# Performance work log

Measured on AMD Instinct MI355X. Metric: run time of the kernel, lower is better.

## Reference

```python
import jax, jax.numpy as jnp
import numpy as np

EMBED_DIMS = 256

def setup_inputs() -> dict:
    key = jax.random.key(0)
    ks = jax.random.split(key, 6)
    C = EMBED_DIMS
    x = jax.random.normal(ks[0], (4, 2048, C), dtype=jnp.float32)
    prev_x = jax.random.normal(ks[1], (4, 2048, C), dtype=jnp.float32)
    s = 1.0 / np.sqrt(C)
    W_qkv = jax.random.uniform(ks[2], (C, 3 * C), dtype=jnp.float32, minval=-s, maxval=s)
    b_qkv = jax.random.uniform(ks[3], (3 * C,), dtype=jnp.float32, minval=-s, maxval=s)
    W_out = jax.random.uniform(ks[4], (C, C), dtype=jnp.float32, minval=-s, maxval=s)
    b_out = jax.random.uniform(ks[5], (C,), dtype=jnp.float32, minval=-s, maxval=s)
    return {"x": x, "prev_x": prev_x, "W_qkv": W_qkv, "b_qkv": b_qkv,
            "W_out": W_out, "b_out": b_out}

def reference(x, prev_x, W_qkv, b_qkv, W_out, b_out):
    B, N, C = x.shape
    xx = jnp.concatenate([prev_x, x], axis=1)          # [B, S, C], S = 2N
    qkv = xx @ W_qkv + b_qkv                            # [B, S, 3C]
    q, k, v = jnp.split(qkv, 3, axis=-1)                # each [B, S, C]
    scale = 1.0 / jnp.sqrt(jnp.asarray(C, dtype=x.dtype))
    attn = jax.nn.softmax(jnp.einsum('bqc,bkc->bqk', q, k) * scale, axis=-1)
    out = jnp.einsum('bqk,bkc->bqc', attn, v)           # [B, S, C]
    out = out @ W_out + b_out
    return out[:, -N:, :]                               # [B, N, C]
```

## Files before the change

kernel.cpp:

```cpp
#include <hip/hip_runtime.h>

typedef __bf16 bf16;
typedef __attribute__((ext_vector_type(8))) __bf16 bf16x8;
typedef __attribute__((ext_vector_type(4))) __bf16 bf16x4;
typedef __attribute__((ext_vector_type(4))) float f32x4;
typedef __attribute__((ext_vector_type(16))) float f32x16;
typedef __attribute__((ext_vector_type(4))) unsigned u32x4;

#define MFMA16(a, b, c) __builtin_amdgcn_mfma_f32_16x16x32_bf16(a, b, c, 0, 0, 0)
#define MFMA32(a, b, c) __builtin_amdgcn_mfma_f32_32x32x16_bf16(a, b, c, 0, 0, 0)

__device__ inline void gload_lds16(const void* g, void* l) {
  __builtin_amdgcn_global_load_lds(
      (const __attribute__((address_space(1))) void*)g,
      (__attribute__((address_space(3))) void*)l, 16, 0, 0);
}

__device__ inline unsigned packbf(float a, float b) {
  unsigned short x = __builtin_bit_cast(unsigned short, (bf16)a);
  unsigned short y = __builtin_bit_cast(unsigned short, (bf16)b);
  return (unsigned)x | ((unsigned)y << 16);
}

__global__ __launch_bounds__(256) void prep_w_kernel(
    const float* __restrict__ Wqkv, const float* __restrict__ Wout,
    bf16* __restrict__ Wqkvt, bf16* __restrict__ Woutt)
{
  int tid = blockIdx.x * 256 + threadIdx.x;
  int nth = gridDim.x * 256;
  for (int i = tid; i < 768 * 256; i += nth) {
    int n = i >> 8, k = i & 255;
    Wqkvt[i] = (bf16)Wqkv[k * 768 + n];
  }
  for (int i = tid; i < 256 * 256; i += nth) {
    int n = i >> 8, k = i & 255;
    Woutt[i] = (bf16)Wout[k * 256 + n];
  }
}

__global__ __launch_bounds__(256) void gemm_qkv_kernel(
    const float* __restrict__ x, const float* __restrict__ px,
    const bf16* __restrict__ Wt, const float* __restrict__ bias,
    bf16* __restrict__ Qo, bf16* __restrict__ KVo)
{
  const int bi = blockIdx.x;
  const int b = bi >> 6;
  const int mblk = bi & 63;
  const bool mhalf = mblk >= 32;
  const int bm = b * 4096 + mblk * 64;
  const int s_local = (mblk & 31) * 64;
  const float* xsrc = mhalf ? x : px;
  const size_t xbase = ((size_t)b << 19) + (size_t)s_local * 256;

  const int tid = threadIdx.x;
  const int lane = tid & 63, w = tid >> 6;
  const int l15 = lane & 15, lg = lane >> 4;

  alignas(16) __shared__ bf16 Alds[64 * 256];
  alignas(16) __shared__ bf16 Wlds[2][256 * 32];

  const int ystart = mhalf ? 0 : 1;
  const int nseq = mhalf ? 24 : 16;

  auto stageW = [&](int i) {
    const int y = ystart + (i >> 3);
    const int k0 = (i & 7) * 32;
    #pragma unroll
    for (int jj = 0; jj < 4; jj++) {
      int j = w * 4 + jj;
      int row = j * 16 + (lane >> 2);
      int chunk = (lane & 3) ^ ((row >> 1) & 3);
      const bf16* g = Wt + (size_t)(y * 256 + row) * 256 + k0 + chunk * 8;
      gload_lds16(g, (char*)&Wlds[i & 1][0] + j * 1024);
    }
  };
  stageW(0);

  #pragma unroll
  for (int it = 0; it < 8; it++) {
    int c = it * 256 + tid;
    int row = c >> 5, ch = c & 31;
    const float* src = xsrc + xbase + (size_t)row * 256 + ch * 8;
    float4 f0 = *(const float4*)src;
    float4 f1 = *(const float4*)(src + 4);
    bf16x8 v = { (bf16)f0.x, (bf16)f0.y, (bf16)f0.z, (bf16)f0.w,
                 (bf16)f1.x, (bf16)f1.y, (bf16)f1.z, (bf16)f1.w };
    *(bf16x8*)((char*)Alds + ((c << 4) ^ ((row & 7) << 4))) = v;
  }
  __syncthreads();

  f32x4 acc[16] = {};
  for (int i = 0; i < nseq; i++) {
    if (i + 1 < nseq) stageW(i + 1);
    const int k0 = (i & 7) * 32;
    const bf16* wbuf = &Wlds[i & 1][0];
    const int arow = w * 16 + l15;
    bf16x8 afr = *(const bf16x8*)((char*)Alds +
        ((arow * 512 + k0 * 2 + lg * 16) ^ ((arow & 7) << 4)));
    #pragma unroll
    for (int nt = 0; nt < 16; nt++) {
      const int wrow = nt * 16 + l15;
      bf16x8 bfr = *(const bf16x8*)((char*)wbuf +
          (((wrow << 6) + (lg << 4)) ^ (((wrow >> 1) & 3) << 4)));
      acc[nt] = MFMA16(afr, bfr, acc[nt]);
    }
    __syncthreads();

    if ((i & 7) == 7) {
      const int y = ystart + (i >> 3);
      const int m0 = bm + w * 16 + lg * 4;
      const int bq = m0 >> 12, s = m0 & 4095;
      #pragma unroll
      for (int nt = 0; nt < 16; nt++) {
        const int n = nt * 16 + l15;
        const float bv = bias[y * 256 + n];
        if (y == 0) {
          const int ks = n >> 4, h2 = (n >> 3) & 1, e = n & 7;
          #pragma unroll
          for (int rr = 0; rr < 4; rr++) {
            const int qrow = bq * 2048 + (s - 2048) + rr;
            Qo[(size_t)(qrow >> 5) * 8192 + ks * 512 +
               ((qrow & 31) + 32 * h2) * 8 + e] =
                (bf16)((acc[nt][rr] + bv) * 0.0625f);
          }
        } else if (y == 1) {
          const int d = n;
          const int ks = d >> 4, h2 = (d >> 3) & 1, e = d & 7;
          const size_t tb = (size_t)(bq * 128 + (s >> 5)) * 16384;
          #pragma unroll
          for (int rr = 0; rr < 4; rr++)
            KVo[tb + ks * 512 + (((s & 31) + rr) + 32 * h2) * 8 + e] =
                (bf16)(acc[nt][rr] + bv);
        } else {
          const int d = n;
          const int kv32 = s & 31;
          const int sidx = kv32 >> 4, h2 = (kv32 >> 3) & 1, e0 = kv32 & 7;
          bf16x4 st = { (bf16)(acc[nt][0] + bv), (bf16)(acc[nt][1] + bv),
                        (bf16)(acc[nt][2] + bv), (bf16)(acc[nt][3] + bv) };
          *(bf16x4*)(KVo + (size_t)(bq * 128 + (s >> 5)) * 16384 + 8192 +
                     (sidx * 8 + (d >> 5)) * 512 + ((d & 31) + 32 * h2) * 8 + e0) = st;
        }
        acc[nt] = (f32x4){};
      }
    }
  }
}

__global__ __launch_bounds__(256, 2) void attn_kernel(
    const bf16* __restrict__ Qp, const bf16* __restrict__ KVp,
    bf16* __restrict__ Opart, float* __restrict__ ml)
{
  const int id = blockIdx.x;
  const int c = id & 7;
  const int b = (id >> 3) & 3;
  const int qb = id >> 5;
  const int tid = threadIdx.x;
  const int lane = tid & 63, w = tid >> 6;
  const int l31 = lane & 31, hi = lane >> 5;

  __shared__ bf16 lds[2][16384];

  const int qg = b * 64 + qb * 4 + w;
  const bf16* qbase = Qp + (size_t)qg * 8192 + lane * 8;
  bf16x8 qf[16];
  #pragma unroll
  for (int ks = 0; ks < 16; ks++)
    qf[ks] = *(const bf16x8*)(qbase + ks * 512);

  const bf16* kvtile0 = KVp + (size_t)(b * 128 + c * 16) * 16384;

  auto stage = [&](int t) {
    const char* g = (const char*)(kvtile0 + (size_t)t * 16384) + w * 8192 + lane * 16;
    char* l = (char*)&lds[t & 1][0] + w * 8192;
    #pragma unroll
    for (int j = 0; j < 8; j++)
      gload_lds16(g + j * 1024, l + j * 1024);
  };
  stage(0);

  f32x16 o[8] = {};
  float m_run = -1e30f, l_run = 0.f;

  for (int t = 0; t < 16; t++) {
    __syncthreads();
    if (t + 1 < 16) stage(t + 1);
    const bf16* kbuf = &lds[t & 1][0];
    const bf16* vbuf = kbuf + 8192;

    f32x16 p = {};
    __builtin_amdgcn_s_setprio(1);
    #pragma unroll
    for (int ks = 0; ks < 16; ks++) {
      bf16x8 kf = *(const bf16x8*)(kbuf + ks * 512 + lane * 8);
      p = MFMA32(kf, qf[ks], p);
    }
    __builtin_amdgcn_s_setprio(0);

    float mt = fmaxf(p[0], p[1]);
    #pragma unroll
    for (int i = 2; i < 16; i++) mt = fmaxf(mt, p[i]);
    mt = fmaxf(mt, __shfl_xor(mt, 32));
    if (!__all(mt <= m_run + 8.f)) {
      const float m_new = fmaxf(m_run, mt);
      const float alpha = __expf(m_run - m_new);
      l_run *= alpha;
      #pragma unroll
      for (int i = 0; i < 8; i++)
        #pragma unroll
        for (int j = 0; j < 16; j++) o[i][j] *= alpha;
      m_run = m_new;
    }
    float ps = 0.f;
    #pragma unroll
    for (int i = 0; i < 16; i++) { p[i] = __expf(p[i] - m_run); ps += p[i]; }
    ps += __shfl_xor(ps, 32);
    l_run += ps;

    unsigned u[8], xp[8];
    #pragma unroll
    for (int i = 0; i < 8; i++) u[i] = packbf(p[2 * i], p[2 * i + 1]);
    #pragma unroll
    for (int i = 0; i < 8; i++)
      xp[i] = (unsigned)__shfl_xor((int)u[i], 32);
    const u32x4 w0 = hi ? (u32x4){xp[2], xp[3], u[2], u[3]}
                        : (u32x4){u[0], u[1], xp[0], xp[1]};
    const u32x4 w1 = hi ? (u32x4){xp[6], xp[7], u[6], u[7]}
                        : (u32x4){u[4], u[5], xp[4], xp[5]};
    const bf16x8 pf0 = __builtin_bit_cast(bf16x8, w0);
    const bf16x8 pf1 = __builtin_bit_cast(bf16x8, w1);

    __builtin_amdgcn_s_setprio(1);
    #pragma unroll
    for (int dg = 0; dg < 8; dg++) {
      bf16x8 v0 = *(const bf16x8*)(vbuf + dg * 512 + lane * 8);
      o[dg] = MFMA32(v0, pf0, o[dg]);
      bf16x8 v1 = *(const bf16x8*)(vbuf + (8 + dg) * 512 + lane * 8);
      o[dg] = MFMA32(v1, pf1, o[dg]);
    }
    __builtin_amdgcn_s_setprio(0);
  }

  const int q = b * 2048 + qb * 128 + w * 32 + l31;
  bf16* ob = Opart + ((size_t)c * 8192 + q) * 256;
  #pragma unroll
  for (int dg = 0; dg < 8; dg++) {
    #pragma unroll
    for (int r4 = 0; r4 < 4; r4++) {
      const int d = dg * 32 + r4 * 8 + hi * 4;
      bf16x4 st = { (bf16)o[dg][r4 * 4 + 0], (bf16)o[dg][r4 * 4 + 1],
                    (bf16)o[dg][r4 * 4 + 2], (bf16)o[dg][r4 * 4 + 3] };
      *(bf16x4*)(ob + d) = st;
    }
  }
  if (hi == 0) {
    float2 v = { m_run, l_run };
    *(float2*)(ml + ((size_t)c * 8192 + q) * 2) = v;
  }
}

__global__ __launch_bounds__(256) void out_kernel(
    const bf16* __restrict__ Opart, const float* __restrict__ ml,
    const bf16* __restrict__ Woutt, const float* __restrict__ bout,
    float* __restrict__ out)
{
  const int bm = blockIdx.x * 32;
  const int tid = threadIdx.x;
  const int lane = tid & 63, w = tid >> 6;
  const int l15 = lane & 15, lg = lane >> 4;

  alignas(16) __shared__ bf16 Alds[32 * 256];
  alignas(16) __shared__ bf16 Wlds[2][256 * 32];

  auto stageW = [&](int k0) {
    #pragma unroll
    for (int jj = 0; jj < 4; jj++) {
      int j = w * 4 + jj;
      int row = j * 16 + (lane >> 2);
      int chunk = (lane & 3) ^ ((row >> 1) & 3);
      const bf16* g = Woutt + (size_t)row * 256 + k0 * 32 + chunk * 8;
      gload_lds16(g, (char*)&Wlds[k0 & 1][0] + j * 1024);
    }
  };
  stageW(0);

  #pragma unroll
  for (int ch = 0; ch < 4; ch++) {
    const int idx = ch * 256 + tid;
    const int row = idx >> 5;
    const int dc = (idx & 31) << 3;
    const int q = bm + row;
    float ms[8], ls[8], M = -1e30f;
    #pragma unroll
    for (int s = 0; s < 8; s++) {
      float2 v = *(const float2*)(ml + ((size_t)s * 8192 + q) * 2);
      ms[s] = v.x; ls[s] = v.y;
      M = fmaxf(M, v.x);
    }
    float L = 0.f, acc[8] = {};
    #pragma unroll
    for (int s = 0; s < 8; s++) {
      const float wgt = __expf(ms[s] - M);
      L += ls[s] * wgt;
      bf16x8 v = *(const bf16x8*)(Opart + ((size_t)s * 8192 + q) * 256 + dc);
      #pragma unroll
      for (int j = 0; j < 8; j++) acc[j] += wgt * (float)v[j];
    }
    const float inv = 1.f / L;
    bf16x8 st;
    #pragma unroll
    for (int j = 0; j < 8; j++) st[j] = (bf16)(acc[j] * inv);
    *(bf16x8*)((char*)Alds + ((row * 512 + dc * 2) ^ ((row & 7) << 4))) = st;
  }
  __syncthreads();

  f32x4 acc[8] = {};
  for (int k0 = 0; k0 < 8; k0++) {
    if (k0 + 1 < 8) stageW(k0 + 1);
    const bf16* wbuf = &Wlds[k0 & 1][0];
    const int arow = (w & 1) * 16 + l15;
    bf16x8 afr = *(const bf16x8*)((char*)Alds +
        ((arow * 512 + k0 * 64 + lg * 16) ^ ((arow & 7) << 4)));
    #pragma unroll
    for (int nt = 0; nt < 8; nt++) {
      const int wrow = (w >> 1) * 128 + nt * 16 + l15;
      bf16x8 bfr = *(const bf16x8*)((char*)wbuf +
          (((wrow << 6) + (lg << 4)) ^ (((wrow >> 1) & 3) << 4)));
      acc[nt] = MFMA16(afr, bfr, acc[nt]);
    }
    __syncthreads();
  }

  #pragma unroll
  for (int nt = 0; nt < 8; nt++) {
    const int n = (w >> 1) * 128 + nt * 16 + l15;
    const float bvv = bout[n];
    const int m0 = bm + (w & 1) * 16 + lg * 4;
    #pragma unroll
    for (int r = 0; r < 4; r++)
      out[(size_t)(m0 + r) * 256 + n] = acc[nt][r] + bvv;
  }
}

extern "C" void kernel_launch(void* const* d_in, const int* in_sizes, int n_in,
                              void* d_out, int out_size, void* d_ws, size_t ws_size,
                              hipStream_t stream) {
  const float* x    = (const float*)d_in[0];
  const float* px   = (const float*)d_in[1];
  const float* Wqkv = (const float*)d_in[2];
  const float* bqkv = (const float*)d_in[3];
  const float* Wout = (const float*)d_in[4];
  const float* bout = (const float*)d_in[5];
  float* out = (float*)d_out;

  char* ws = (char*)d_ws;
  bf16* Qp    = (bf16*)(ws);
  bf16* KVp   = (bf16*)(ws + 4194304);
  bf16* Woutt = (bf16*)(ws + 20971520);
  bf16* Wqkvt = (bf16*)(ws + 21102592);
  float* ml   = (float*)(ws + 21495808);
  bf16* Opart = (bf16*)(ws + 22020096);

  prep_w_kernel<<<dim3(128), dim3(256), 0, stream>>>(Wqkv, Wout, Wqkvt, Woutt);
  gemm_qkv_kernel<<<dim3(256), dim3(256), 0, stream>>>(
      x, px, Wqkvt, bqkv, Qp, KVp);
  attn_kernel<<<dim3(512), dim3(256), 0, stream>>>(Qp, KVp, Opart, ml);
  out_kernel<<<dim3(256), dim3(256), 0, stream>>>(Opart, ml, Woutt, bout, out);
}
```

Measured before the change: 104.7 us.

## Split QKV GEMM across output projections into 640 blocks with per-k staging

The QKV projection kernel used to launch one block per 64-row tile, and each block looped over two or three output projections (K,V or Q,K,V). Now each block handles one (row tile, projection) pair, giving 640 blocks and better balance across CUs. The A tile is loaded per 32-wide k slice instead of once for the full 256 width, and W is no longer double-buffered. LDS use drops, which may allow more resident blocks, but each block now re-reads and re-converts x for every projection and has no overlap between loads and MFMA.

```diff
diff --git a/kernel.cpp b/kernel.cpp
--- a/kernel.cpp
+++ b/kernel.cpp
@@ -43,105 +43,91 @@
     const bf16* __restrict__ Wt, const float* __restrict__ bias,
     bf16* __restrict__ Qo, bf16* __restrict__ KVo)
 {
-  const int bi = blockIdx.x;
-  const int b = bi >> 6;
-  const int mblk = bi & 63;
-  const bool mhalf = mblk >= 32;
+  const int idb = blockIdx.x;
+  const int b = idb / 160;
+  const int r = idb % 160;
+  int mblk, y;
+  if (r < 64) { mblk = r >> 1; y = 1 + (r & 1); }
+  else { int r2 = r - 64; mblk = 32 + r2 / 3; y = r2 % 3; }
   const int bm = b * 4096 + mblk * 64;
-  const int s_local = (mblk & 31) * 64;
-  const float* xsrc = mhalf ? x : px;
-  const size_t xbase = ((size_t)b << 19) + (size_t)s_local * 256;
 
   const int tid = threadIdx.x;
   const int lane = tid & 63, w = tid >> 6;
   const int l15 = lane & 15, lg = lane >> 4;
 
-  alignas(16) __shared__ bf16 Alds[64 * 256];
-  alignas(16) __shared__ bf16 Wlds[2][256 * 32];
-
-  const int ystart = mhalf ? 0 : 1;
-  const int nseq = mhalf ? 24 : 16;
-
-  auto stageW = [&](int i) {
-    const int y = ystart + (i >> 3);
-    const int k0 = (i & 7) * 32;
+  alignas(16) __shared__ bf16 Alds[64 * 32];
+  alignas(16) __shared__ bf16 Wlds[256 * 32];
+
+  f32x4 acc[16] = {};
+
+  const float* xsrc = (mblk >= 32) ? x : px;
+  const size_t xbase = ((size_t)b << 19) + (size_t)((mblk & 31) * 64) * 256;
+
+  for (int k0 = 0; k0 < 256; k0 += 32) {
+    __syncthreads();
+    {
+      int c = tid;
+      int row = c >> 2, kc = (c & 3) << 3;
+      const float* src = xsrc + xbase + (size_t)row * 256 + k0 + kc;
+      float4 f0 = *(const float4*)src;
+      float4 f1 = *(const float4*)(src + 4);
+      bf16x8 v = { (bf16)f0.x, (bf16)f0.y, (bf16)f0.z, (bf16)f0.w,
+                   (bf16)f1.x, (bf16)f1.y, (bf16)f1.z, (bf16)f1.w };
+      *(bf16x8*)((char*)Alds + ((c << 4) ^ (((row >> 1) & 3) << 4))) = v;
+    }
     #pragma unroll
     for (int jj = 0; jj < 4; jj++) {
       int j = w * 4 + jj;
       int row = j * 16 + (lane >> 2);
       int chunk = (lane & 3) ^ ((row >> 1) & 3);
       const bf16* g = Wt + (size_t)(y * 256 + row) * 256 + k0 + chunk * 8;
-      gload_lds16(g, (char*)&Wlds[i & 1][0] + j * 1024);
-    }
-  };
-  stageW(0);
-
-  #pragma unroll
-  for (int it = 0; it < 8; it++) {
-    int c = it * 256 + tid;
-    int row = c >> 5, ch = c & 31;
-    const float* src = xsrc + xbase + (size_t)row * 256 + ch * 8;
-    float4 f0 = *(const float4*)src;
-    float4 f1 = *(const float4*)(src + 4);
-    bf16x8 v = { (bf16)f0.x, (bf16)f0.y, (bf16)f0.z, (bf16)f0.w,
-                 (bf16)f1.x, (bf16)f1.y, (bf16)f1.z, (bf16)f1.w };
-    *(bf16x8*)((char*)Alds + ((c << 4) ^ ((row & 7) << 4))) = v;
-  }
-  __syncthreads();
-
-  f32x4 acc[16] = {};
-  for (int i = 0; i < nseq; i++) {
-    if (i + 1 < nseq) stageW(i + 1);
-    const int k0 = (i & 7) * 32;
-    const bf16* wbuf = &Wlds[i & 1][0];
+      gload_lds16(g, (char*)Wlds + j * 1024);
+    }
+    __syncthreads();
+
     const int arow = w * 16 + l15;
     bf16x8 afr = *(const bf16x8*)((char*)Alds +
-        ((arow * 512 + k0 * 2 + lg * 16) ^ ((arow & 7) << 4)));
+        (((arow << 6) + (lg << 4)) ^ (((arow >> 1) & 3) << 4)));
     #pragma unroll
     for (int nt = 0; nt < 16; nt++) {
       const int wrow = nt * 16 + l15;
-      bf16x8 bfr = *(const bf16x8*)((char*)wbuf +
+      bf16x8 bfr = *(const bf16x8*)((char*)Wlds +
           (((wrow << 6) + (lg << 4)) ^ (((wrow >> 1) & 3) << 4)));
       acc[nt] = MFMA16(afr, bfr, acc[nt]);
     }
-    __syncthreads();
-
-    if ((i & 7) == 7) {
-      const int y = ystart + (i >> 3);
-      const int m0 = bm + w * 16 + lg * 4;
-      const int bq = m0 >> 12, s = m0 & 4095;
+  }
+
+  const int m0 = bm + w * 16 + lg * 4;
+  const int bq = m0 >> 12, s = m0 & 4095;
+  #pragma unroll
+  for (int nt = 0; nt < 16; nt++) {
+    const int n = nt * 16 + l15;
+    const float bv = bias[y * 256 + n];
+    if (y == 0) {
+      const int ks = n >> 4, h2 = (n >> 3) & 1, e = n & 7;
       #pragma unroll
-      for (int nt = 0; nt < 16; nt++) {
-        const int n = nt * 16 + l15;
-        const float bv = bias[y * 256 + n];
-        if (y == 0) {
-          const int ks = n >> 4, h2 = (n >> 3) & 1, e = n & 7;
-          #pragma unroll
-          for (int rr = 0; rr < 4; rr++) {
-            const int qrow = bq * 2048 + (s - 2048) + rr;
-            Qo[(size_t)(qrow >> 5) * 8192 + ks * 512 +
-               ((qrow & 31) + 32 * h2) * 8 + e] =
-                (bf16)((acc[nt][rr] + bv) * 0.0625f);
-          }
-        } else if (y == 1) {
-          const int d = n;
-          const int ks = d >> 4, h2 = (d >> 3) & 1, e = d & 7;
-          const size_t tb = (size_t)(bq * 128 + (s >> 5)) * 16384;
-          #pragma unroll
-          for (int rr = 0; rr < 4; rr++)
-            KVo[tb + ks * 512 + (((s & 31) + rr) + 32 * h2) * 8 + e] =
-                (bf16)(acc[nt][rr] + bv);
-        } else {
-          const int d = n;
-          const int kv32 = s & 31;
-          const int sidx = kv32 >> 4, h2 = (kv32 >> 3) & 1, e0 = kv32 & 7;
-          bf16x4 st = { (bf16)(acc[nt][0] + bv), (bf16)(acc[nt][1] + bv),
-                        (bf16)(acc[nt][2] + bv), (bf16)(acc[nt][3] + bv) };
-          *(bf16x4*)(KVo + (size_t)(bq * 128 + (s >> 5)) * 16384 + 8192 +
-                     (sidx * 8 + (d >> 5)) * 512 + ((d & 31) + 32 * h2) * 8 + e0) = st;
-        }
-        acc[nt] = (f32x4){};
+      for (int rr = 0; rr < 4; rr++) {
+        const int qrow = bq * 2048 + (s - 2048) + rr;
+        Qo[(size_t)(qrow >> 5) * 8192 + ks * 512 +
+           ((qrow & 31) + 32 * h2) * 8 + e] =
+            (bf16)((acc[nt][rr] + bv) * 0.0625f);
       }
+    } else if (y == 1) {
+      const int d = n;
+      const int ks = d >> 4, h2 = (d >> 3) & 1, e = d & 7;
+      const size_t tb = (size_t)(bq * 128 + (s >> 5)) * 16384;
+      #pragma unroll
+      for (int rr = 0; rr < 4; rr++)
+        KVo[tb + ks * 512 + (((s & 31) + rr) + 32 * h2) * 8 + e] =
+            (bf16)(acc[nt][rr] + bv);
+    } else {
+      const int d = n;
+      const int kv32 = s & 31;
+      const int sidx = kv32 >> 4, h2 = (kv32 >> 3) & 1, e0 = kv32 & 7;
+      bf16x4 st = { (bf16)(acc[nt][0] + bv), (bf16)(acc[nt][1] + bv),
+                    (bf16)(acc[nt][2] + bv), (bf16)(acc[nt][3] + bv) };
+      *(bf16x4*)(KVo + (size_t)(bq * 128 + (s >> 5)) * 16384 + 8192 +
+                 (sidx * 8 + (d >> 5)) * 512 + ((d & 31) + 32 * h2) * 8 + e0) = st;
     }
   }
 }
@@ -361,7 +347,7 @@
   bf16* Opart = (bf16*)(ws + 22020096);
 
   prep_w_kernel<<<dim3(128), dim3(256), 0, stream>>>(Wqkv, Wout, Wqkvt, Woutt);
-  gemm_qkv_kernel<<<dim3(256), dim3(256), 0, stream>>>(
+  gemm_qkv_kernel<<<dim3(640), dim3(256), 0, stream>>>(
       x, px, Wqkvt, bqkv, Qp, KVp);
   attn_kernel<<<dim3(512), dim3(256), 0, stream>>>(Qp, KVp, Opart, ml);
   out_kernel<<<dim3(256), dim3(256), 0, stream>>>(Opart, ml, Woutt, bout, out);
```

Result: faster. 88.85 us (-15.1%).

## Halve QKV GEMM row tiles, split warps over N, and break attention MFMA dependency chains

Applied to the files above, without the earlier changes.

The QKV projection now uses 32-row blocks with twice as many blocks, and each wave covers a 64-column slice for both 16-row halves instead of a 16-row slice across all columns. This gives better CU occupancy and reuses each W fragment across two A fragments. In attention, the QK^T reduction is split into four independent accumulators, and the max and sum reductions become trees, which shortens serial dependency chains. In exchange there are more accumulator registers, extra adds, and W tiles re-streamed from memory by twice as many blocks.

```diff
diff --git a/kernel.cpp b/kernel.cpp
--- a/kernel.cpp
+++ b/kernel.cpp
@@ -43,24 +43,24 @@
     const bf16* __restrict__ Wt, const float* __restrict__ bias,
     bf16* __restrict__ Qo, bf16* __restrict__ KVo)
 {
-  const int bi = blockIdx.x;
-  const int b = bi >> 6;
-  const int mblk = bi & 63;
-  const bool mhalf = mblk >= 32;
-  const int bm = b * 4096 + mblk * 64;
-  const int s_local = (mblk & 31) * 64;
-  const float* xsrc = mhalf ? x : px;
-  const size_t xbase = ((size_t)b << 19) + (size_t)s_local * 256;
+  const int id = blockIdx.x;
+  const int b = id >> 7;
+  const int r = id & 127;
+  const bool mhigh = r >= 64;
+  const int mblk = r & 63;
+  const int bm = b * 4096 + (mhigh ? 2048 : 0) + mblk * 32;
+  const float* xsrc = mhigh ? x : px;
+  const size_t xbase = ((size_t)b << 19) + (size_t)(mblk * 32) * 256;
 
   const int tid = threadIdx.x;
   const int lane = tid & 63, w = tid >> 6;
   const int l15 = lane & 15, lg = lane >> 4;
 
-  alignas(16) __shared__ bf16 Alds[64 * 256];
+  alignas(16) __shared__ bf16 Alds[32 * 256];
   alignas(16) __shared__ bf16 Wlds[2][256 * 32];
 
-  const int ystart = mhalf ? 0 : 1;
-  const int nseq = mhalf ? 24 : 16;
+  const int ystart = mhigh ? 0 : 1;
+  const int nseq = mhigh ? 24 : 16;
 
   auto stageW = [&](int i) {
     const int y = ystart + (i >> 3);
@@ -77,7 +77,7 @@
   stageW(0);
 
   #pragma unroll
-  for (int it = 0; it < 8; it++) {
+  for (int it = 0; it < 4; it++) {
     int c = it * 256 + tid;
     int row = c >> 5, ch = c & 31;
     const float* src = xsrc + xbase + (size_t)row * 256 + ch * 8;
@@ -89,58 +89,69 @@
   }
   __syncthreads();
 
-  f32x4 acc[16] = {};
+  f32x4 acc[8] = {};
   for (int i = 0; i < nseq; i++) {
     if (i + 1 < nseq) stageW(i + 1);
     const int k0 = (i & 7) * 32;
     const bf16* wbuf = &Wlds[i & 1][0];
-    const int arow = w * 16 + l15;
-    bf16x8 afr = *(const bf16x8*)((char*)Alds +
-        ((arow * 512 + k0 * 2 + lg * 16) ^ ((arow & 7) << 4)));
-    #pragma unroll
-    for (int nt = 0; nt < 16; nt++) {
-      const int wrow = nt * 16 + l15;
+    bf16x8 af0, af1;
+    {
+      const int ar0 = l15;
+      af0 = *(const bf16x8*)((char*)Alds +
+          ((ar0 * 512 + k0 * 2 + lg * 16) ^ ((ar0 & 7) << 4)));
+      const int ar1 = 16 + l15;
+      af1 = *(const bf16x8*)((char*)Alds +
+          ((ar1 * 512 + k0 * 2 + lg * 16) ^ ((ar1 & 7) << 4)));
+    }
+    #pragma unroll
+    for (int nt = 0; nt < 4; nt++) {
+      const int wrow = w * 64 + nt * 16 + l15;
       bf16x8 bfr = *(const bf16x8*)((char*)wbuf +
           (((wrow << 6) + (lg << 4)) ^ (((wrow >> 1) & 3) << 4)));
-      acc[nt] = MFMA16(afr, bfr, acc[nt]);
+      acc[nt] = MFMA16(af0, bfr, acc[nt]);
+      acc[4 + nt] = MFMA16(af1, bfr, acc[4 + nt]);
     }
     __syncthreads();
 
     if ((i & 7) == 7) {
       const int y = ystart + (i >> 3);
-      const int m0 = bm + w * 16 + lg * 4;
-      const int bq = m0 >> 12, s = m0 & 4095;
       #pragma unroll
-      for (int nt = 0; nt < 16; nt++) {
-        const int n = nt * 16 + l15;
-        const float bv = bias[y * 256 + n];
-        if (y == 0) {
-          const int ks = n >> 4, h2 = (n >> 3) & 1, e = n & 7;
-          #pragma unroll
-          for (int rr = 0; rr < 4; rr++) {
-            const int qrow = bq * 2048 + (s - 2048) + rr;
-            Qo[(size_t)(qrow >> 5) * 8192 + ks * 512 +
-               ((qrow & 31) + 32 * h2) * 8 + e] =
-                (bf16)((acc[nt][rr] + bv) * 0.0625f);
+      for (int mt = 0; mt < 2; mt++) {
+        const int m0 = bm + mt * 16 + lg * 4;
+        const int bq = m0 >> 12, s = m0 & 4095;
+        #pragma unroll
+        for (int nt = 0; nt < 4; nt++) {
+          const int ai = mt * 4 + nt;
+          const int n = w * 64 + nt * 16 + l15;
+          const float bv = bias[y * 256 + n];
+          if (y == 0) {
+            const int ks = n >> 4, h2 = (n >> 3) & 1, e = n & 7;
+            #pragma unroll
+            for (int rr = 0; rr < 4; rr++) {
+              const int qrow = bq * 2048 + (s - 2048) + rr;
+              Qo[(size_t)(qrow >> 5) * 8192 + ks * 512 +
+                 ((qrow & 31) + 32 * h2) * 8 + e] =
+                  (bf16)((acc[ai][rr] + bv) * 0.0625f);
+            }
+          } else if (y == 1) {
+            const int d = n;
+            const int ks = d >> 4, h2 = (d >> 3) & 1, e = d & 7;
+            const size_t tb = (size_t)(bq * 128 + (s >> 5)) * 16384;
+            #pragma unroll
+            for (int rr = 0; rr < 4; rr++)
+              KVo[tb + ks * 512 + (((s & 31) + rr) + 32 * h2) * 8 + e] =
+                  (bf16)(acc[ai][rr] + bv);
+          } else {
+            const int d = n;
+            const int kv32 = s & 31;
+            const int sidx = kv32 >> 4, h2 = (kv32 >> 3) & 1, e0 = kv32 & 7;
+            bf16x4 st = { (bf16)(acc[ai][0] + bv), (bf16)(acc[ai][1] + bv),
+                          (bf16)(acc[ai][2] + bv), (bf16)(acc[ai][3] + bv) };
+            *(bf16x4*)(KVo + (size_t)(bq * 128 + (s >> 5)) * 16384 + 8192 +
+                       (sidx * 8 + (d >> 5)) * 512 + ((d & 31) + 32 * h2) * 8 + e0) = st;
           }
-        } else if (y == 1) {
-          const int d = n;
-          const int ks = d >> 4, h2 = (d >> 3) & 1, e = d & 7;
-          const size_t tb = (size_t)(bq * 128 + (s >> 5)) * 16384;
-          #pragma unroll
-          for (int rr = 0; rr < 4; rr++)
-            KVo[tb + ks * 512 + (((s & 31) + rr) + 32 * h2) * 8 + e] =
-                (bf16)(acc[nt][rr] + bv);
-        } else {
-          const int d = n;
-          const int kv32 = s & 31;
-          const int sidx = kv32 >> 4, h2 = (kv32 >> 3) & 1, e0 = kv32 & 7;
-          bf16x4 st = { (bf16)(acc[nt][0] + bv), (bf16)(acc[nt][1] + bv),
-                        (bf16)(acc[nt][2] + bv), (bf16)(acc[nt][3] + bv) };
-          *(bf16x4*)(KVo + (size_t)(bq * 128 + (s >> 5)) * 16384 + 8192 +
-                     (sidx * 8 + (d >> 5)) * 512 + ((d & 31) + 32 * h2) * 8 + e0) = st;
+          acc[ai] = (f32x4){};
         }
-        acc[nt] = (f32x4){};
       }
     }
   }
@@ -187,18 +198,28 @@
     const bf16* kbuf = &lds[t & 1][0];
     const bf16* vbuf = kbuf + 8192;
 
-    f32x16 p = {};
+    f32x16 p0 = {}, p1 = {}, p2 = {}, p3 = {};
     __builtin_amdgcn_s_setprio(1);
     #pragma unroll
-    for (int ks = 0; ks < 16; ks++) {
-      bf16x8 kf = *(const bf16x8*)(kbuf + ks * 512 + lane * 8);
-      p = MFMA32(kf, qf[ks], p);
+    for (int ks = 0; ks < 4; ks++) {
+      bf16x8 kf0 = *(const bf16x8*)(kbuf + ks * 512 + lane * 8);
+      p0 = MFMA32(kf0, qf[ks], p0);
+      bf16x8 kf1 = *(const bf16x8*)(kbuf + (4 + ks) * 512 + lane * 8);
+      p1 = MFMA32(kf1, qf[4 + ks], p1);
+      bf16x8 kf2 = *(const bf16x8*)(kbuf + (8 + ks) * 512 + lane * 8);
+      p2 = MFMA32(kf2, qf[8 + ks], p2);
+      bf16x8 kf3 = *(const bf16x8*)(kbuf + (12 + ks) * 512 + lane * 8);
+      p3 = MFMA32(kf3, qf[12 + ks], p3);
     }
     __builtin_amdgcn_s_setprio(0);
-
-    float mt = fmaxf(p[0], p[1]);
-    #pragma unroll
-    for (int i = 2; i < 16; i++) mt = fmaxf(mt, p[i]);
+    f32x16 p = (p0 + p1) + (p2 + p3);
+
+    float m0 = fmaxf(p[0], p[1]),   m1 = fmaxf(p[2], p[3]);
+    float m2 = fmaxf(p[4], p[5]),   m3 = fmaxf(p[6], p[7]);
+    float m4 = fmaxf(p[8], p[9]),   m5 = fmaxf(p[10], p[11]);
+    float m6 = fmaxf(p[12], p[13]), m7 = fmaxf(p[14], p[15]);
+    m0 = fmaxf(m0, m1); m2 = fmaxf(m2, m3); m4 = fmaxf(m4, m5); m6 = fmaxf(m6, m7);
+    float mt = fmaxf(fmaxf(m0, m2), fmaxf(m4, m6));
     mt = fmaxf(mt, __shfl_xor(mt, 32));
     if (!__all(mt <= m_run + 8.f)) {
       const float m_new = fmaxf(m_run, mt);
@@ -210,9 +231,13 @@
         for (int j = 0; j < 16; j++) o[i][j] *= alpha;
       m_run = m_new;
     }
-    float ps = 0.f;
-    #pragma unroll
-    for (int i = 0; i < 16; i++) { p[i] = __expf(p[i] - m_run); ps += p[i]; }
+    #pragma unroll
+    for (int i = 0; i < 16; i++) p[i] = __expf(p[i] - m_run);
+    float s0 = (p[0] + p[1]) + (p[2] + p[3]);
+    float s1 = (p[4] + p[5]) + (p[6] + p[7]);
+    float s2 = (p[8] + p[9]) + (p[10] + p[11]);
+    float s3 = (p[12] + p[13]) + (p[14] + p[15]);
+    float ps = (s0 + s1) + (s2 + s3);
     ps += __shfl_xor(ps, 32);
     l_run += ps;
 
@@ -361,7 +386,7 @@
   bf16* Opart = (bf16*)(ws + 22020096);
 
   prep_w_kernel<<<dim3(128), dim3(256), 0, stream>>>(Wqkv, Wout, Wqkvt, Woutt);
-  gemm_qkv_kernel<<<dim3(256), dim3(256), 0, stream>>>(
+  gemm_qkv_kernel<<<dim3(512), dim3(256), 0, stream>>>(
       x, px, Wqkvt, bqkv, Qp, KVp);
   attn_kernel<<<dim3(512), dim3(256), 0, stream>>>(Qp, KVp, Opart, ml);
   out_kernel<<<dim3(256), dim3(256), 0, stream>>>(Opart, ml, Woutt, bout, out);
```

After: 103.6 us. No clear change (-1.1%).
